# Kernel optimization log

Measured on AMD Instinct MI355X. Metric: run time of the kernel, lower is better.

## Reference

```python
import jax, jax.numpy as jnp
import numpy as np

N_PARENTS = 4096   # parent clusters
K = 32             # points decoded per cluster
NEIGH = 128        # neigh_dec_size
FEAT = 256         # input_size (per-parent feature dim passed through)


def setup_inputs() -> dict:
    key = jax.random.key(0)
    ks = jax.random.split(key, 6)
    def lin(k, fan_in, fan_out):
        return jax.random.normal(k, (fan_in, fan_out), jnp.float32) / np.sqrt(fan_in).astype(np.float32)
    return {
        "input_features": jax.random.normal(ks[0], (N_PARENTS, NEIGH + FEAT), jnp.float32),
        # neighborhood decoder: Linear NEIGH -> K*3 (relative points)
        "W_dec": lin(ks[1], NEIGH, K * 3), "b_dec": jnp.zeros((K * 3,), jnp.float32),
        # fc chain: (FEAT+3) -> 512 -> 512 -> 256
        "W1": lin(ks[2], FEAT + 3, 512), "b1": jnp.zeros((512,), jnp.float32),
        "W2": lin(ks[3], 512, 512),      "b2": jnp.zeros((512,), jnp.float32),
        "W3": lin(ks[4], 512, 256),      "b3": jnp.zeros((256,), jnp.float32),
    }


def reference(input_features, W_dec, b_dec, W1, b1, W2, b2, W3, b3):
    # split: first NEIGH dims go to the neighborhood decoder, rest are parent features
    neigh_feats = input_features[:, :NEIGH]            # [N, NEIGH]
    features = input_features[:, NEIGH:]               # [N, FEAT]

    # neighborhood_dec: decode K relative 3D points per parent + cluster assignment
    relative_points = (neigh_feats @ W_dec + b_dec).reshape(-1, 3)   # [N*K, 3]
    cluster = jnp.repeat(jnp.arange(N_PARENTS, dtype=jnp.int32), K)  # [N*K]

    # gather parent features per point, concat with relative points
    features_dup = features[cluster]                                  # [N*K, FEAT]
    h = jnp.concatenate([features_dup, relative_points], axis=1)      # [N*K, FEAT+3]

    # chained Linear + ReLU (leaky=False)
    h = jax.nn.relu(h @ W1 + b1)
    h = jax.nn.relu(h @ W2 + b2)
    h = jax.nn.relu(h @ W3 + b3)
    return relative_points, h, cluster
```

## Files before the change

### kernel.cpp

```cpp
#include <hip/hip_runtime.h>
#include <hip/hip_bf16.h>

typedef unsigned short u16;
typedef unsigned int   u32;

#define NP     4096
#define NCH    131072
#define HBASE  393216
#define CLBASE 33947648

#define WS_W2F   0
#define WS_W3F   524288
#define WS_F1    1048576

using bf16x8 = __attribute__((ext_vector_type(8))) short;
using f32x4  = __attribute__((ext_vector_type(4))) float;

__device__ inline u32 pk2(float a, float b) {
  __hip_bfloat162 h = __float22bfloat162_rn(make_float2(a, b));
  return *reinterpret_cast<u32*>(&h);
}

__device__ inline int swz(int r, int cg) {
  return cg ^ (r & 7) ^ ((r >> 3) & 3);
}

__global__ __launch_bounds__(512, 2) void k_pre(const float* __restrict__ in_feats,
                                                const float* __restrict__ Wd,
                                                const float* __restrict__ bd,
                                                const float* __restrict__ W1,
                                                const float* __restrict__ b1,
                                                const float* __restrict__ W2,
                                                const float* __restrict__ W3,
                                                u16* __restrict__ w2f,
                                                u16* __restrict__ w3f,
                                                float* __restrict__ F1,
                                                float* __restrict__ out) {
  __shared__ __align__(16) char smem[51584];
  int b = blockIdx.x, tid = threadIdx.x;

  if (b < 256) {
    u16*   sh_a = (u16*)smem;
    float* b1s  = (float*)(smem + 8192);
    int p0 = b * 16, lane = tid & 63, w = tid >> 6;
    b1s[tid] = b1[tid];
    {
      int r = tid >> 5, k0 = (tid & 31) * 8;
      const float4 v0 = *(const float4*)(in_feats + (p0 + r) * 384 + 128 + k0);
      const float4 v1 = *(const float4*)(in_feats + (p0 + r) * 384 + 128 + k0 + 4);
      uint4 o;
      o.x = pk2(v0.x, v0.y); o.y = pk2(v0.z, v0.w);
      o.z = pk2(v1.x, v1.y); o.w = pk2(v1.z, v1.w);
      int slot = (k0 >> 3) ^ (r & 7);
      *(uint4*)(sh_a + r * 256 + slot * 8) = o;
    }
    __syncthreads();
    f32x4 acc[4];
#pragma unroll
    for (int i = 0; i < 4; ++i) acc[i] = f32x4{0.f, 0.f, 0.f, 0.f};
    int col = lane & 15, q = lane >> 4, q8 = q * 8;
#pragma unroll
    for (int kc = 0; kc < 8; ++kc) {
      int slot = ((kc * 32 + q8) >> 3) ^ (col & 7);
      bf16x8 a = *(const bf16x8*)(sh_a + col * 256 + slot * 8);
#pragma unroll
      for (int nf = 0; nf < 4; ++nf) {
        const float* wp = W1 + (kc * 32 + q8) * 512 + (w * 4 + nf) * 16 + col;
        float v0 = wp[0],      v1 = wp[512],  v2 = wp[1024], v3 = wp[1536];
        float v4 = wp[2048],   v5 = wp[2560], v6 = wp[3072], v7 = wp[3584];
        union { bf16x8 v; u32 u[4]; } uu;
        uu.u[0] = pk2(v0, v1); uu.u[1] = pk2(v2, v3);
        uu.u[2] = pk2(v4, v5); uu.u[3] = pk2(v6, v7);
        acc[nf] = __builtin_amdgcn_mfma_f32_16x16x32_bf16(a, uu.v, acc[nf], 0, 0, 0);
      }
    }
    int rb = (lane >> 4) * 4;
#pragma unroll
    for (int nf = 0; nf < 4; ++nf) {
      int n = w * 64 + nf * 16 + col;
#pragma unroll
      for (int i = 0; i < 4; ++i)
        F1[(p0 + rb + i) * 512 + n] = acc[nf][i] + b1s[n];
    }
  } else if (b < 1280) {
    float* wd  = (float*)smem;
    float* ne  = (float*)(smem + 49152);
    float* bds = (float*)(smem + 51200);
    int p0 = (b - 256) * 4, t = tid;
#pragma unroll
    for (int i = 0; i < 6; ++i)
      *(float4*)(wd + (i * 512 + t) * 4) = *(const float4*)(Wd + (i * 512 + t) * 4);
    { int pp = t >> 7, k = t & 127; ne[t] = in_feats[(p0 + pp) * 384 + k]; }
    if (t < 96) bds[t] = bd[t];
    __syncthreads();
    if (t < 384) {
      int pp = t / 96, c = t - pp * 96;
      float acc = bds[c];
      const float* nep = ne + pp * 128;
#pragma unroll 4
      for (int k = 0; k < 128; ++k) acc += nep[k] * wd[k * 96 + c];
      out[(p0 + pp) * 96 + c] = acc;
    }
  } else if (b < 1472) {
    float (*tile)[32][33] = (float (*)[32][33])smem;
    int h = tid >> 8, t = tid & 255;
    const float* src; u16* dst; int pitchN, g;
    if (b < 1408) { g = (b - 1280) * 2 + h; src = W2; dst = w2f; pitchN = 512; }
    else          { g = (b - 1408) * 2 + h; src = W3; dst = w3f; pitchN = 256; }
    int kt = g & 15, nt = g >> 4;
    {
      int kk = t >> 3, n4 = (t & 7) * 4;
      const float4 v = *(const float4*)(src + (kt * 32 + kk) * pitchN + nt * 32 + n4);
      tile[h][kk][n4 + 0] = v.x; tile[h][kk][n4 + 1] = v.y;
      tile[h][kk][n4 + 2] = v.z; tile[h][kk][n4 + 3] = v.w;
    }
    __syncthreads();
    {
      int s = t >> 1, half = t & 1, fr = s >> 6, l = s & 63;
      int n_l = fr * 16 + (l & 15);
      int k_l = (l >> 4) * 8 + half * 4;
      uint2 o;
      o.x = pk2(tile[h][k_l + 0][n_l], tile[h][k_l + 1][n_l]);
      o.y = pk2(tile[h][k_l + 2][n_l], tile[h][k_l + 3][n_l]);
      int frag_id = (nt * 2 + fr) * 16 + kt;
      *(uint2*)(dst + frag_id * 512 + l * 8 + half * 4) = o;
    }
  } else {
    int idx = ((b - 1472) * 512 + tid) * 4;
    float c = (float)(idx >> 5);
    float* p = out + CLBASE + idx;
    __builtin_nontemporal_store(c, p + 0);
    __builtin_nontemporal_store(c, p + 1);
    __builtin_nontemporal_store(c, p + 2);
    __builtin_nontemporal_store(c, p + 3);
  }
}

__global__ __launch_bounds__(512, 2) void k_main(const float* __restrict__ W1,
                                                 const float* __restrict__ b2,
                                                 const float* __restrict__ b3,
                                                 const u16* __restrict__ w2f,
                                                 const u16* __restrict__ w3f,
                                                 const float* __restrict__ F1,
                                                 float* __restrict__ out) {
  int blk = blockIdx.x;
  int tid = threadIdx.x, lane = tid & 63, w = tid >> 6;
  __shared__ u16 sh_h[128 * 512];
  __shared__ float f1s[2048], w1bs[1536], b2s[512], b3s[256], rels[384];

  *(float4*)(f1s + tid * 4) = *(const float4*)(F1 + blk * 2048 + tid * 4);
  w1bs[tid]        = W1[131072 + tid];
  w1bs[tid + 512]  = W1[131072 + 512 + tid];
  w1bs[tid + 1024] = W1[131072 + 1024 + tid];
  b2s[tid] = b2[tid];
  if (tid < 256) b3s[tid] = b3[tid];
  if (tid < 384) rels[tid] = out[blk * 384 + tid];
  __syncthreads();

  {
    int r = tid & 31, g = tid >> 5;
#pragma unroll
    for (int rr = 0; rr < 128; rr += 32) {
      int row = rr + r, pp = rr >> 5;
      float r0 = rels[row * 3 + 0], r1 = rels[row * 3 + 1], r2 = rels[row * 3 + 2];
#pragma unroll
      for (int gg = 0; gg < 4; ++gg) {
        int c8 = g * 8 + gg * 128;
        const float4 fa = *(const float4*)(f1s + pp * 512 + c8);
        const float4 fb = *(const float4*)(f1s + pp * 512 + c8 + 4);
        const float4 wa0 = *(const float4*)(w1bs + c8);
        const float4 wb0 = *(const float4*)(w1bs + c8 + 4);
        const float4 wa1 = *(const float4*)(w1bs + 512 + c8);
        const float4 wb1 = *(const float4*)(w1bs + 512 + c8 + 4);
        const float4 wa2 = *(const float4*)(w1bs + 1024 + c8);
        const float4 wb2 = *(const float4*)(w1bs + 1024 + c8 + 4);
        float v0 = fmaxf(fa.x + r0 * wa0.x + r1 * wa1.x + r2 * wa2.x, 0.f);
        float v1 = fmaxf(fa.y + r0 * wa0.y + r1 * wa1.y + r2 * wa2.y, 0.f);
        float v2 = fmaxf(fa.z + r0 * wa0.z + r1 * wa1.z + r2 * wa2.z, 0.f);
        float v3 = fmaxf(fa.w + r0 * wa0.w + r1 * wa1.w + r2 * wa2.w, 0.f);
        float v4 = fmaxf(fb.x + r0 * wb0.x + r1 * wb1.x + r2 * wb2.x, 0.f);
        float v5 = fmaxf(fb.y + r0 * wb0.y + r1 * wb1.y + r2 * wb2.y, 0.f);
        float v6 = fmaxf(fb.z + r0 * wb0.z + r1 * wb1.z + r2 * wb2.z, 0.f);
        float v7 = fmaxf(fb.w + r0 * wb0.w + r1 * wb1.w + r2 * wb2.w, 0.f);
        uint4 o;
        o.x = pk2(v0, v1); o.y = pk2(v2, v3);
        o.z = pk2(v4, v5); o.w = pk2(v6, v7);
        *(uint4*)(sh_h + row * 512 + swz(row, c8 >> 3) * 8) = o;
      }
    }
  }
  __syncthreads();

  int col = lane & 15, q8 = (lane >> 4) * 8;

  f32x4 acc2[8][4];
#pragma unroll
  for (int mf = 0; mf < 8; ++mf)
#pragma unroll
    for (int nf = 0; nf < 4; ++nf) acc2[mf][nf] = f32x4{0.f, 0.f, 0.f, 0.f};
  {
    const u16* w2p = w2f + (size_t)(w * 4 * 16) * 512 + lane * 8;
    bf16x8 bufA[4], bufB[4];
#pragma unroll
    for (int nf = 0; nf < 4; ++nf) bufA[nf] = *(const bf16x8*)(w2p + nf * 16 * 512);
#pragma unroll 2
    for (int kc = 0; kc < 16; ++kc) {
      const bf16x8* cur = (kc & 1) ? bufB : bufA;
      bf16x8* nxt = (kc & 1) ? bufA : bufB;
      if (kc < 15) {
#pragma unroll
        for (int nf = 0; nf < 4; ++nf)
          nxt[nf] = *(const bf16x8*)(w2p + (nf * 16 + kc + 1) * 512);
      }
      int cb = (kc * 32 + q8) >> 3;
#pragma unroll
      for (int mf = 0; mf < 8; ++mf) {
        int row = mf * 16 + col;
        bf16x8 a = *(const bf16x8*)(sh_h + row * 512 + swz(row, cb) * 8);
#pragma unroll
        for (int nf = 0; nf < 4; ++nf)
          acc2[mf][nf] = __builtin_amdgcn_mfma_f32_16x16x32_bf16(a, cur[nf], acc2[mf][nf], 0, 0, 0);
      }
    }
  }
  __syncthreads();

  {
    int rq = (lane >> 4) * 4;
#pragma unroll
    for (int mf = 0; mf < 8; ++mf)
#pragma unroll
      for (int nf = 0; nf < 4; ++nf) {
        int n = w * 64 + nf * 16 + col, cg = n >> 3, n7 = n & 7;
        float bv = b2s[n];
#pragma unroll
        for (int i = 0; i < 4; i += 2) {
          int r0 = mf * 16 + rq + i, r1 = r0 + 1;
          u32 p = pk2(fmaxf(acc2[mf][nf][i] + bv, 0.f),
                      fmaxf(acc2[mf][nf][i + 1] + bv, 0.f));
          sh_h[r0 * 512 + swz(r0, cg) * 8 + n7] = (u16)(p & 0xffff);
          sh_h[r1 * 512 + swz(r1, cg) * 8 + n7] = (u16)(p >> 16);
        }
      }
  }
  __syncthreads();

  f32x4 acc3[8][2];
#pragma unroll
  for (int mf = 0; mf < 8; ++mf)
#pragma unroll
    for (int nf = 0; nf < 2; ++nf) acc3[mf][nf] = f32x4{0.f, 0.f, 0.f, 0.f};
  {
    const u16* w3p = w3f + (size_t)(w * 2 * 16) * 512 + lane * 8;
    bf16x8 bufA[2], bufB[2];
#pragma unroll
    for (int nf = 0; nf < 2; ++nf) bufA[nf] = *(const bf16x8*)(w3p + nf * 16 * 512);
#pragma unroll 2
    for (int kc = 0; kc < 16; ++kc) {
      const bf16x8* cur = (kc & 1) ? bufB : bufA;
      bf16x8* nxt = (kc & 1) ? bufA : bufB;
      if (kc < 15) {
#pragma unroll
        for (int nf = 0; nf < 2; ++nf)
          nxt[nf] = *(const bf16x8*)(w3p + (nf * 16 + kc + 1) * 512);
      }
      int cb = (kc * 32 + q8) >> 3;
#pragma unroll
      for (int mf = 0; mf < 8; ++mf) {
        int row = mf * 16 + col;
        bf16x8 a = *(const bf16x8*)(sh_h + row * 512 + swz(row, cb) * 8);
#pragma unroll
        for (int nf = 0; nf < 2; ++nf)
          acc3[mf][nf] = __builtin_amdgcn_mfma_f32_16x16x32_bf16(a, cur[nf], acc3[mf][nf], 0, 0, 0);
      }
    }
  }

  {
    int rq = (lane >> 4) * 4;
#pragma unroll
    for (int mf = 0; mf < 8; ++mf)
#pragma unroll
      for (int nf = 0; nf < 2; ++nf) {
        int n = w * 32 + nf * 16 + col;
        float bv = b3s[n];
#pragma unroll
        for (int i = 0; i < 4; ++i) {
          int r = mf * 16 + rq + i;
          float v = fmaxf(acc3[mf][nf][i] + bv, 0.f);
          __builtin_nontemporal_store(v, out + HBASE + (blk * 128 + r) * 256 + n);
        }
      }
  }
}

extern "C" void kernel_launch(void* const* d_in, const int* in_sizes, int n_in,
                              void* d_out, int out_size, void* d_ws, size_t ws_size,
                              hipStream_t stream) {
  const float* in_feats = (const float*)d_in[0];
  const float* Wd = (const float*)d_in[1];
  const float* bd = (const float*)d_in[2];
  const float* W1 = (const float*)d_in[3];
  const float* b1 = (const float*)d_in[4];
  const float* W2 = (const float*)d_in[5];
  const float* b2 = (const float*)d_in[6];
  const float* W3 = (const float*)d_in[7];
  const float* b3 = (const float*)d_in[8];
  float* out = (float*)d_out;
  char* ws = (char*)d_ws;
  u16*   w2f = (u16*)(ws + WS_W2F);
  u16*   w3f = (u16*)(ws + WS_W3F);
  float* F1  = (float*)(ws + WS_F1);

  k_pre<<<1536, 512, 0, stream>>>(in_feats, Wd, bd, W1, b1, W2, W3, w2f, w3f, F1, out);
  k_main<<<1024, 512, 0, stream>>>(W1, b2, b3, w2f, w3f, F1, out);
}
```

Measured before the change: 276.2 us.

## Fuse neighborhood decoder into F1 blocks and halve k_main rows per block

The relative-point decoder moves into the same k_pre blocks that compute the first-layer parent features, using a transposed Wd in shared memory and float4 dot products. This removes 1024 separate decoder blocks and the redundant per-block load of all of Wd. k_main now processes 64 rows (2 parents) per block instead of 128, halving shared memory and accumulator registers so the launch bound can request 4 blocks per CU, across 2048 blocks. The trade-off is less reuse of each W2/W3 fragment load per block and larger shared memory in k_pre.

```diff
diff --git a/kernel.cpp b/kernel.cpp
--- a/kernel.cpp
+++ b/kernel.cpp
@@ -36,14 +36,22 @@
                                                 u16* __restrict__ w3f,
                                                 float* __restrict__ F1,
                                                 float* __restrict__ out) {
-  __shared__ __align__(16) char smem[51584];
+  __shared__ __align__(16) char smem[69504];
   int b = blockIdx.x, tid = threadIdx.x;
 
   if (b < 256) {
     u16*   sh_a = (u16*)smem;
     float* b1s  = (float*)(smem + 8192);
+    float* wdT  = (float*)(smem + 10240);
+    float* ne   = (float*)(smem + 60928);
+    float* bds  = (float*)(smem + 69120);
     int p0 = b * 16, lane = tid & 63, w = tid >> 6;
     b1s[tid] = b1[tid];
+    if (tid < 96) bds[tid] = bd[tid];
+    {
+      int r = tid >> 5, k4 = (tid & 31) * 4;
+      *(float4*)(ne + r * 128 + k4) = *(const float4*)(in_feats + (p0 + r) * 384 + k4);
+    }
     {
       int r = tid >> 5, k0 = (tid & 31) * 8;
       const float4 v0 = *(const float4*)(in_feats + (p0 + r) * 384 + 128 + k0);
@@ -54,11 +62,38 @@
       int slot = (k0 >> 3) ^ (r & 7);
       *(uint4*)(sh_a + r * 256 + slot * 8) = o;
     }
+    {
+#pragma unroll
+      for (int i = 0; i < 6; ++i) {
+        int idx = i * 512 + tid;
+        int k = idx / 24, c4 = (idx % 24) * 4;
+        const float4 v = *(const float4*)(Wd + k * 96 + c4);
+        wdT[(c4 + 0) * 132 + k] = v.x;
+        wdT[(c4 + 1) * 132 + k] = v.y;
+        wdT[(c4 + 2) * 132 + k] = v.z;
+        wdT[(c4 + 3) * 132 + k] = v.w;
+      }
+    }
     __syncthreads();
+#pragma unroll
+    for (int j = 0; j < 3; ++j) {
+      int u = j * 512 + tid;
+      int p = u / 96, c = u - p * 96;
+      const float4* nep = (const float4*)(ne + p * 128);
+      const float4* wp  = (const float4*)(wdT + c * 132);
+      float4 a4 = {0.f, 0.f, 0.f, 0.f};
+#pragma unroll 8
+      for (int kq = 0; kq < 32; ++kq) {
+        const float4 av = nep[kq], bv = wp[kq];
+        a4.x += av.x * bv.x; a4.y += av.y * bv.y;
+        a4.z += av.z * bv.z; a4.w += av.w * bv.w;
+      }
+      out[(p0 + p) * 96 + c] = bds[c] + ((a4.x + a4.y) + (a4.z + a4.w));
+    }
     f32x4 acc[4];
 #pragma unroll
     for (int i = 0; i < 4; ++i) acc[i] = f32x4{0.f, 0.f, 0.f, 0.f};
-    int col = lane & 15, q = lane >> 4, q8 = q * 8;
+    int col = lane & 15, q8 = (lane >> 4) * 8;
 #pragma unroll
     for (int kc = 0; kc < 8; ++kc) {
       int slot = ((kc * 32 + q8) >> 3) ^ (col & 7);
@@ -82,31 +117,12 @@
       for (int i = 0; i < 4; ++i)
         F1[(p0 + rb + i) * 512 + n] = acc[nf][i] + b1s[n];
     }
-  } else if (b < 1280) {
-    float* wd  = (float*)smem;
-    float* ne  = (float*)(smem + 49152);
-    float* bds = (float*)(smem + 51200);
-    int p0 = (b - 256) * 4, t = tid;
-#pragma unroll
-    for (int i = 0; i < 6; ++i)
-      *(float4*)(wd + (i * 512 + t) * 4) = *(const float4*)(Wd + (i * 512 + t) * 4);
-    { int pp = t >> 7, k = t & 127; ne[t] = in_feats[(p0 + pp) * 384 + k]; }
-    if (t < 96) bds[t] = bd[t];
-    __syncthreads();
-    if (t < 384) {
-      int pp = t / 96, c = t - pp * 96;
-      float acc = bds[c];
-      const float* nep = ne + pp * 128;
-#pragma unroll 4
-      for (int k = 0; k < 128; ++k) acc += nep[k] * wd[k * 96 + c];
-      out[(p0 + pp) * 96 + c] = acc;
-    }
-  } else if (b < 1472) {
+  } else if (b < 448) {
     float (*tile)[32][33] = (float (*)[32][33])smem;
     int h = tid >> 8, t = tid & 255;
     const float* src; u16* dst; int pitchN, g;
-    if (b < 1408) { g = (b - 1280) * 2 + h; src = W2; dst = w2f; pitchN = 512; }
-    else          { g = (b - 1408) * 2 + h; src = W3; dst = w3f; pitchN = 256; }
+    if (b < 384) { g = (b - 256) * 2 + h; src = W2; dst = w2f; pitchN = 512; }
+    else         { g = (b - 384) * 2 + h; src = W3; dst = w3f; pitchN = 256; }
     int kt = g & 15, nt = g >> 4;
     {
       int kk = t >> 3, n4 = (t & 7) * 4;
@@ -126,7 +142,7 @@
       *(uint2*)(dst + frag_id * 512 + l * 8 + half * 4) = o;
     }
   } else {
-    int idx = ((b - 1472) * 512 + tid) * 4;
+    int idx = ((b - 448) * 512 + tid) * 4;
     float c = (float)(idx >> 5);
     float* p = out + CLBASE + idx;
     __builtin_nontemporal_store(c, p + 0);
@@ -136,7 +152,7 @@
   }
 }
 
-__global__ __launch_bounds__(512, 2) void k_main(const float* __restrict__ W1,
+__global__ __launch_bounds__(512, 4) void k_main(const float* __restrict__ W1,
                                                  const float* __restrict__ b2,
                                                  const float* __restrict__ b3,
                                                  const u16* __restrict__ w2f,
@@ -145,22 +161,23 @@
                                                  float* __restrict__ out) {
   int blk = blockIdx.x;
   int tid = threadIdx.x, lane = tid & 63, w = tid >> 6;
-  __shared__ u16 sh_h[128 * 512];
-  __shared__ float f1s[2048], w1bs[1536], b2s[512], b3s[256], rels[384];
-
-  *(float4*)(f1s + tid * 4) = *(const float4*)(F1 + blk * 2048 + tid * 4);
+  __shared__ u16 sh_h[64 * 512];
+  __shared__ float f1s[1024], w1bs[1536], b2s[512], b3s[256], rels[192];
+
+  f1s[tid]       = F1[blk * 1024 + tid];
+  f1s[tid + 512] = F1[blk * 1024 + 512 + tid];
   w1bs[tid]        = W1[131072 + tid];
   w1bs[tid + 512]  = W1[131072 + 512 + tid];
   w1bs[tid + 1024] = W1[131072 + 1024 + tid];
   b2s[tid] = b2[tid];
   if (tid < 256) b3s[tid] = b3[tid];
-  if (tid < 384) rels[tid] = out[blk * 384 + tid];
+  if (tid < 192) rels[tid] = out[blk * 192 + tid];
   __syncthreads();
 
   {
     int r = tid & 31, g = tid >> 5;
 #pragma unroll
-    for (int rr = 0; rr < 128; rr += 32) {
+    for (int rr = 0; rr < 64; rr += 32) {
       int row = rr + r, pp = rr >> 5;
       float r0 = rels[row * 3 + 0], r1 = rels[row * 3 + 1], r2 = rels[row * 3 + 2];
 #pragma unroll
@@ -193,9 +210,9 @@
 
   int col = lane & 15, q8 = (lane >> 4) * 8;
 
-  f32x4 acc2[8][4];
-#pragma unroll
-  for (int mf = 0; mf < 8; ++mf)
+  f32x4 acc2[4][4];
+#pragma unroll
+  for (int mf = 0; mf < 4; ++mf)
 #pragma unroll
     for (int nf = 0; nf < 4; ++nf) acc2[mf][nf] = f32x4{0.f, 0.f, 0.f, 0.f};
   {
@@ -214,7 +231,7 @@
       }
       int cb = (kc * 32 + q8) >> 3;
 #pragma unroll
-      for (int mf = 0; mf < 8; ++mf) {
+      for (int mf = 0; mf < 4; ++mf) {
         int row = mf * 16 + col;
         bf16x8 a = *(const bf16x8*)(sh_h + row * 512 + swz(row, cb) * 8);
 #pragma unroll
@@ -228,7 +245,7 @@
   {
     int rq = (lane >> 4) * 4;
 #pragma unroll
-    for (int mf = 0; mf < 8; ++mf)
+    for (int mf = 0; mf < 4; ++mf)
 #pragma unroll
       for (int nf = 0; nf < 4; ++nf) {
         int n = w * 64 + nf * 16 + col, cg = n >> 3, n7 = n & 7;
@@ -245,9 +262,9 @@
   }
   __syncthreads();
 
-  f32x4 acc3[8][2];
-#pragma unroll
-  for (int mf = 0; mf < 8; ++mf)
+  f32x4 acc3[4][2];
+#pragma unroll
+  for (int mf = 0; mf < 4; ++mf)
 #pragma unroll
     for (int nf = 0; nf < 2; ++nf) acc3[mf][nf] = f32x4{0.f, 0.f, 0.f, 0.f};
   {
@@ -266,7 +283,7 @@
       }
       int cb = (kc * 32 + q8) >> 3;
 #pragma unroll
-      for (int mf = 0; mf < 8; ++mf) {
+      for (int mf = 0; mf < 4; ++mf) {
         int row = mf * 16 + col;
         bf16x8 a = *(const bf16x8*)(sh_h + row * 512 + swz(row, cb) * 8);
 #pragma unroll
@@ -279,7 +296,7 @@
   {
     int rq = (lane >> 4) * 4;
 #pragma unroll
-    for (int mf = 0; mf < 8; ++mf)
+    for (int mf = 0; mf < 4; ++mf)
 #pragma unroll
       for (int nf = 0; nf < 2; ++nf) {
         int n = w * 32 + nf * 16 + col;
@@ -288,7 +305,7 @@
         for (int i = 0; i < 4; ++i) {
           int r = mf * 16 + rq + i;
           float v = fmaxf(acc3[mf][nf][i] + bv, 0.f);
-          __builtin_nontemporal_store(v, out + HBASE + (blk * 128 + r) * 256 + n);
+          __builtin_nontemporal_store(v, out + HBASE + (blk * 64 + r) * 256 + n);
         }
       }
   }
@@ -312,6 +329,6 @@
   u16*   w3f = (u16*)(ws + WS_W3F);
   float* F1  = (float*)(ws + WS_F1);
 
-  k_pre<<<1536, 512, 0, stream>>>(in_feats, Wd, bd, W1, b1, W2, W3, w2f, w3f, F1, out);
-  k_main<<<1024, 512, 0, stream>>>(W1, b2, b3, w2f, w3f, F1, out);
-}
+  k_pre<<<512, 512, 0, stream>>>(in_feats, Wd, bd, W1, b1, W2, W3, w2f, w3f, F1, out);
+  k_main<<<2048, 512, 0, stream>>>(W1, b2, b3, w2f, w3f, F1, out);
+}
```

New measurement: 317.5 us. 1.15x slower.
